# Kernel tuning notes

Hardware: AMD Instinct MI355X
Metric: run time of the kernel (lower is better)

Reference implementation:

```python
import jax, jax.numpy as jnp
import numpy as np

B, S, D, H = 2, 2048, 2048, 16
DH = D // H            # 128 head dim
QP = D // 2            # 1024 compressed q dim
KVP = (2 * D) // 3     # 1365 compressed kv dim
RD = DH // 2           # 64 rope dim
ND = DH // 2           # 64 nope dim
FF = 4 * D
THETA = 10000.0


def _ln(x, w, b, eps=1e-5):
    m = jnp.mean(x, -1, keepdims=True)
    v = jnp.mean((x - m) ** 2, -1, keepdims=True)
    return (x - m) * jax.lax.rsqrt(v + eps) * w + b


def _rotate_half(x):
    x1, x2 = jnp.split(x, 2, axis=-1)
    return jnp.concatenate([-x2, x1], axis=-1)


def setup_inputs() -> dict:
    key = jax.random.key(0)
    ks = jax.random.split(key, 9)
    rn = lambda k, shp, s: (s * jax.random.normal(k, shp)).astype(jnp.float32)
    return {
        'x': jax.random.normal(ks[0], (B, S, D), jnp.float32),
        'attn_norm_w': jnp.ones((D,), jnp.float32), 'attn_norm_b': jnp.zeros((D,), jnp.float32),
        'W_dq': rn(ks[1], (D, QP), 0.01),
        'q_ln_w': jnp.ones((QP,), jnp.float32), 'q_ln_b': jnp.zeros((QP,), jnp.float32),
        'W_uq': rn(ks[2], (QP, D), 0.01),
        'W_dkv': rn(ks[3], (D, KVP + RD), 0.01),
        'kv_ln_w': jnp.ones((KVP,), jnp.float32), 'kv_ln_b': jnp.zeros((KVP,), jnp.float32),
        'W_ukv': rn(ks[4], (KVP, D + H * ND), 0.01),
        'W_o': rn(ks[5], (D, D), 0.01),
        'ff_norm_w': jnp.ones((D,), jnp.float32), 'ff_norm_b': jnp.zeros((D,), jnp.float32),
        'W1': rn(ks[6], (D, FF), 0.02), 'b1': jnp.zeros((FF,), jnp.float32),
        'W2': rn(ks[7], (FF, D), 0.02), 'b2': jnp.zeros((D,), jnp.float32),
    }


def reference(x, attn_norm_w, attn_norm_b, W_dq, q_ln_w, q_ln_b, W_uq, W_dkv,
              kv_ln_w, kv_ln_b, W_ukv, W_o, ff_norm_w, ff_norm_b, W1, b1, W2, b2):
    # ---- pre-LN attention ----
    h = _ln(x, attn_norm_w, attn_norm_b)
    # Q path: down-proj, LN, up-proj
    cq = _ln(h @ W_dq, q_ln_w, q_ln_b)                      # [B,S,QP]
    Q = (cq @ W_uq).reshape(B, S, H, DH).transpose(0, 2, 1, 3)  # [B,H,S,DH]
    Qn, Qr = Q[..., :ND], Q[..., ND:]
    # RoPE tables: emb [S, DH/2]; take first RD/2 freqs, tile -> [1,1,S,RD]
    pos = jnp.arange(S, dtype=jnp.float32)
    freqs = 1.0 / (THETA ** (jnp.arange(0, DH, 2, dtype=jnp.float32) / DH))
    emb = pos[:, None] * freqs[None, :]
    cos = jnp.tile(jnp.cos(emb)[:, :RD // 2], (1, 2))[None, None]
    sin = jnp.tile(jnp.sin(emb)[:, :RD // 2], (1, 2))[None, None]
    Qr = Qr * cos + _rotate_half(Qr) * sin
    # KV path: joint down-proj, split latent / shared rope key
    ckv = h @ W_dkv                                          # [B,S,KVP+RD]
    kv_lora, k_rope = ckv[..., :KVP], ckv[..., KVP:]
    kv_lora = _ln(kv_lora, kv_ln_w, kv_ln_b)
    KV = (kv_lora @ W_ukv).reshape(B, S, H, DH + ND).transpose(0, 2, 1, 3)
    K, V = KV[..., :ND], KV[..., ND:]                        # K [B,H,S,ND], V [B,H,S,DH]
    Kr = k_rope[:, None]                                     # [B,1,S,RD] shared across heads
    Kr = Kr * cos + _rotate_half(Kr) * sin
    Kr = jnp.broadcast_to(Kr, (B, H, S, RD))
    q = jnp.concatenate([Qn, Qr], -1)                        # [B,H,S,DH]
    k = jnp.concatenate([K, Kr], -1)                         # [B,H,S,DH]
    scores = jnp.einsum('bhqd,bhkd->bhqk', q, k) / jnp.sqrt(jnp.float32(DH))
    mask = jnp.tril(jnp.ones((S, S), bool))
    scores = jnp.where(mask, scores, jnp.finfo(scores.dtype).min)
    attn = jax.nn.softmax(scores, axis=-1)
    o = jnp.einsum('bhqk,bhkd->bhqd', attn, V).transpose(0, 2, 1, 3).reshape(B, S, D)
    o = o @ W_o.T
    x = x + o  # dropout is identity at eval
    # ---- pre-LN MLP ----
    r = x
    h = _ln(x, ff_norm_w, ff_norm_b)
    h = jax.nn.gelu(h @ W1 + b1, approximate=False) @ W2 + b2
    return r + h, ckv
```

## Files before the change

kernel.cpp:

```cpp
#include <hip/hip_runtime.h>
#include <hip/hip_bf16.h>
#include <math.h>

#define B_ 2
#define S_ 2048
#define D_ 2048
#define H_ 16
#define DH_ 128
#define QP_ 1024
#define KVP_ 1365
#define RD_ 64
#define ND_ 64
#define FF_ 8192
#define T_ (B_*S_)
#define CKW_ (KVP_+RD_)
#define KVW_ 3072
#define KVP_PAD 1408
#define CKW_PAD 1536

typedef __attribute__((ext_vector_type(8))) short short8;
typedef __attribute__((ext_vector_type(4))) short sh4;
typedef __attribute__((ext_vector_type(4))) float floatx4;

__device__ __forceinline__ void gload_lds16(const __hip_bfloat16* g, __hip_bfloat16* l) {
    __builtin_amdgcn_global_load_lds((const __attribute__((address_space(1))) void*)g,
                                     (__attribute__((address_space(3))) void*)l, 16, 0, 0);
}
__device__ __forceinline__ short f2bs(float f) {
    __hip_bfloat16 h = __float2bfloat16(f);
    return *reinterpret_cast<short*>(&h);
}
__device__ __forceinline__ int sw(int row, int g) { return row * 64 + ((g ^ (row & 7)) << 3); }

__device__ __forceinline__ float fast_gelu(float v) {
    float x = v * 0.70710678118654752f;
    float ax = fabsf(x);
    float t = __builtin_amdgcn_rcpf(1.f + 0.3275911f * ax);
    float y = t * (0.254829592f + t * (-0.284496736f + t * (1.421413741f + t * (-1.453152027f + t * 1.061405429f))));
    float e = __expf(-ax * ax);
    float erfv = 1.f - y * e;
    erfv = copysignf(erfv, x);
    return 0.5f * v * (1.f + erfv);
}

__global__ __launch_bounds__(256) void ln_bf16(const float* __restrict__ in, int in_stride,
                                               const float* __restrict__ w, const float* __restrict__ bb,
                                               __hip_bfloat16* __restrict__ out, int out_stride, int N)
{
    int row = blockIdx.x;
    const float* ip = in + (size_t)row * in_stride;
    __hip_bfloat16* op = out + (size_t)row * out_stride;
    int tid = threadIdx.x;
    float sum = 0.f, sq = 0.f;
    for (int i = tid; i < N; i += 256) { float v = ip[i]; sum += v; sq += v * v; }
    __shared__ float s1[256], s2[256];
    s1[tid] = sum; s2[tid] = sq; __syncthreads();
    for (int s = 128; s > 0; s >>= 1) {
        if (tid < s) { s1[tid] += s1[tid + s]; s2[tid] += s2[tid + s]; }
        __syncthreads();
    }
    float mean = s1[0] / N;
    float var  = s2[0] / N - mean * mean;
    float rstd = rsqrtf(var + 1e-5f);
    for (int i = tid; i < N; i += 256) {
        float v = ip[i];
        op[i] = __float2bfloat16((v - mean) * rstd * w[i] + bb[i]);
    }
    for (int i = N + tid; i < out_stride; i += 256) op[i] = __float2bfloat16(0.f);
}

__global__ __launch_bounds__(256) void transpose_cvt(const float* __restrict__ W, __hip_bfloat16* __restrict__ Wt,
                                                     int K, int N, int Kp)
{
    __shared__ float t[32][33];
    int k0 = blockIdx.x * 32, n0 = blockIdx.y * 32;
    int tx = threadIdx.x & 31, ty = threadIdx.x >> 5;
    for (int r = ty; r < 32; r += 8) {
        int k = k0 + r, n = n0 + tx;
        t[r][tx] = (k < K && n < N) ? W[(size_t)k * N + n] : 0.f;
    }
    __syncthreads();
    for (int r = ty; r < 32; r += 8) {
        int n = n0 + r, k = k0 + tx;
        Wt[(size_t)n * Kp + k] = __float2bfloat16(t[tx][r]);
    }
}

__global__ __launch_bounds__(256) void cvt_bf16(const float* __restrict__ in, __hip_bfloat16* __restrict__ out, int n)
{
    int i = blockIdx.x * 256 + threadIdx.x;
    if (i < n) out[i] = __float2bfloat16(in[i]);
}

template<int EPI, typename CT>
__global__ __launch_bounds__(256) void gemm_bf16(const __hip_bfloat16* __restrict__ A,
                                                 const __hip_bfloat16* __restrict__ Bt,
                                                 CT* __restrict__ C, int M, int N, int Kp, int ldc,
                                                 const float* __restrict__ bias,
                                                 const float* __restrict__ resid)
{
    __shared__ __hip_bfloat16 As[128 * 64];
    __shared__ __hip_bfloat16 Bs[128 * 64];
    int tid = threadIdx.x;
    int bm = blockIdx.y * 128;
    int bn = blockIdx.x * 128;
    int wid = tid >> 6, lane = tid & 63;
    int wm = (wid >> 1) * 64, wn = (wid & 1) * 64;
    int lrow = lane & 15;
    int quad = lane >> 4;

    floatx4 acc[4][4];
    #pragma unroll
    for (int i = 0; i < 4; ++i)
        #pragma unroll
        for (int j = 0; j < 4; ++j)
            acc[i][j] = (floatx4){0.f, 0.f, 0.f, 0.f};

    for (int k0 = 0; k0 < Kp; k0 += 64) {
        #pragma unroll
        for (int it = 0; it < 4; ++it) {
            int chunk = it * 256 + tid;
            int row = chunk >> 3, g = chunk & 7;
            int col = (g ^ (row & 7)) << 3;
            gload_lds16(A + (size_t)(bm + row) * Kp + k0 + col, &As[chunk * 8]);
        }
        #pragma unroll
        for (int it = 0; it < 4; ++it) {
            int chunk = it * 256 + tid;
            int row = chunk >> 3, g = chunk & 7;
            int col = (g ^ (row & 7)) << 3;
            gload_lds16(Bt + (size_t)(bn + row) * Kp + k0 + col, &Bs[chunk * 8]);
        }
        __syncthreads();
        #pragma unroll
        for (int kk = 0; kk < 2; ++kk) {
            short8 a[4], b[4];
            #pragma unroll
            for (int i = 0; i < 4; ++i)
                a[i] = *(const short8*)&As[sw(wm + i * 16 + lrow, kk * 4 + quad)];
            #pragma unroll
            for (int j = 0; j < 4; ++j)
                b[j] = *(const short8*)&Bs[sw(wn + j * 16 + lrow, kk * 4 + quad)];
            #pragma unroll
            for (int i = 0; i < 4; ++i)
                #pragma unroll
                for (int j = 0; j < 4; ++j)
                    acc[i][j] = __builtin_amdgcn_mfma_f32_16x16x32_bf16(a[i], b[j], acc[i][j], 0, 0, 0);
        }
        __syncthreads();
    }

    int cq4 = quad * 4;
    #pragma unroll
    for (int i = 0; i < 4; ++i) {
        #pragma unroll
        for (int j = 0; j < 4; ++j) {
            int col = bn + wn + j * 16 + lrow;
            if (col >= N) continue;
            #pragma unroll
            for (int r = 0; r < 4; ++r) {
                int rowg = bm + wm + i * 16 + cq4 + r;
                float v = acc[i][j][r];
                size_t idx = (size_t)rowg * ldc + col;
                if (EPI == 1) v += resid[idx];
                if (EPI == 2) { v += bias[col]; v = fast_gelu(v); }
                if (EPI == 3) { v += bias[col]; v += ((const float*)C)[idx]; }
                C[idx] = (CT)v;
            }
        }
    }
}

__global__ __launch_bounds__(256) void rope_q_kernel(float* __restrict__ Q)
{
    int idx = blockIdx.x * 256 + threadIdx.x;
    int i = idx & 31;
    int h = (idx >> 5) & (H_ - 1);
    int t = idx >> 9;
    float f = expf(-(float)i * (9.210340371976184f / 64.0f));
    float ang = (float)(t & (S_ - 1)) * f;
    float sv, cv; sincosf(ang, &sv, &cv);
    float* p = Q + (size_t)t * D_ + h * DH_ + ND_;
    float u = p[i], v = p[i + 32];
    p[i]      = u * cv - v * sv;
    p[i + 32] = v * cv + u * sv;
}

__global__ __launch_bounds__(256) void rope_kr_bf(const float* __restrict__ ckv, __hip_bfloat16* __restrict__ kr)
{
    int idx = blockIdx.x * 256 + threadIdx.x;
    int i = idx & 31;
    int t = idx >> 5;
    float f = expf(-(float)i * (9.210340371976184f / 64.0f));
    float ang = (float)(t & (S_ - 1)) * f;
    float sv, cv; sincosf(ang, &sv, &cv);
    const float* src = ckv + (size_t)t * CKW_ + KVP_;
    float u = src[i], v = src[i + 32];
    kr[(size_t)t * RD_ + i]      = __float2bfloat16(u * cv - v * sv);
    kr[(size_t)t * RD_ + i + 32] = __float2bfloat16(v * cv + u * sv);
}

__global__ __launch_bounds__(256) void vt_pack(const __hip_bfloat16* __restrict__ kvu,
                                               __hip_bfloat16* __restrict__ Vt)
{
    int bh = blockIdx.y; int b = bh >> 4, h = bh & 15;
    int v = threadIdx.x & 127;
    int tg = blockIdx.x * 2 + (threadIdx.x >> 7);
    int t0 = tg * 8;
    short8 o;
    #pragma unroll
    for (int j = 0; j < 8; ++j) {
        __hip_bfloat16 e = kvu[(size_t)(b * S_ + t0 + j) * KVW_ + h * 192 + 64 + v];
        o[j] = *reinterpret_cast<short*>(&e);
    }
    *(short8*)&Vt[((size_t)bh * 128 + v) * S_ + t0] = o;
}

__global__ __launch_bounds__(256) void attn_mfma(const float* __restrict__ Q,
                                                 const __hip_bfloat16* __restrict__ KVU,
                                                 const __hip_bfloat16* __restrict__ KR,
                                                 const __hip_bfloat16* __restrict__ VT,
                                                 __hip_bfloat16* __restrict__ O)
{
    __shared__ __hip_bfloat16 Kls[64 * 64];
    __shared__ __hip_bfloat16 Krls[64 * 64];
    __shared__ __hip_bfloat16 Vls[128 * 64];
    __shared__ __hip_bfloat16 Pls[4 * 32 * 64];

    int tid = threadIdx.x, wid = tid >> 6, lane = tid & 63;
    int lrow = lane & 15, quad = lane >> 4;
    int kq8 = quad * 8;
    int qtile = 15 - blockIdx.x;
    int bh = blockIdx.y, b = bh >> 4, h = bh & 15;
    int q0 = qtile * 128, wq = wid * 32;

    const float scale = 0.08838834764831845f;

    short8 bq[2][2], bqr[2][2];
    #pragma unroll
    for (int n = 0; n < 2; ++n) {
        const float* qrow = Q + (size_t)(b * S_ + q0 + wq + n * 16 + lrow) * D_ + h * DH_;
        #pragma unroll
        for (int s = 0; s < 2; ++s) {
            int base = s * 32 + kq8;
            #pragma unroll
            for (int j = 0; j < 8; ++j) {
                bq[n][s][j]  = f2bs(qrow[base + j] * scale);
                bqr[n][s][j] = f2bs(qrow[64 + base + j] * scale);
            }
        }
    }

    float mstate[2] = {-INFINITY, -INFINITY};
    float lstate[2] = {0.f, 0.f};
    floatx4 acco[8][2];
    #pragma unroll
    for (int vt = 0; vt < 8; ++vt)
        #pragma unroll
        for (int n = 0; n < 2; ++n)
            acco[vt][n] = (floatx4){0.f, 0.f, 0.f, 0.f};

    int nk = qtile * 2 + 2;
    int qmax_w = q0 + wq + 31;

    for (int kt = 0; kt < nk; ++kt) {
        int k0 = kt * 64;
        #pragma unroll
        for (int it = 0; it < 2; ++it) {
            int c = it * 256 + tid;
            int row = c >> 3, g = c & 7;
            int col = ((g ^ (row & 7)) << 3);
            gload_lds16(KVU + (size_t)(b * S_ + k0 + row) * KVW_ + h * 192 + col, &Kls[c * 8]);
            gload_lds16(KR + (size_t)(b * S_ + k0 + row) * RD_ + col, &Krls[c * 8]);
        }
        #pragma unroll
        for (int it = 0; it < 4; ++it) {
            int c = it * 256 + tid;
            int row = c >> 3, g = c & 7;
            int col = ((g ^ (row & 7)) << 3);
            gload_lds16(VT + ((size_t)bh * 128 + row) * S_ + k0 + col, &Vls[c * 8]);
        }
        __syncthreads();

        if (k0 <= qmax_w) {
            floatx4 sacc[4][2];
            #pragma unroll
            for (int m = 0; m < 4; ++m)
                #pragma unroll
                for (int n = 0; n < 2; ++n)
                    sacc[m][n] = (floatx4){0.f, 0.f, 0.f, 0.f};
            #pragma unroll
            for (int m = 0; m < 4; ++m) {
                short8 ak[2], akr[2];
                #pragma unroll
                for (int s = 0; s < 2; ++s) {
                    ak[s]  = *(const short8*)&Kls[sw(m * 16 + lrow, s * 4 + quad)];
                    akr[s] = *(const short8*)&Krls[sw(m * 16 + lrow, s * 4 + quad)];
                }
                #pragma unroll
                for (int n = 0; n < 2; ++n)
                    #pragma unroll
                    for (int s = 0; s < 2; ++s) {
                        sacc[m][n] = __builtin_amdgcn_mfma_f32_16x16x32_bf16(ak[s],  bq[n][s],  sacc[m][n], 0, 0, 0);
                        sacc[m][n] = __builtin_amdgcn_mfma_f32_16x16x32_bf16(akr[s], bqr[n][s], sacc[m][n], 0, 0, 0);
                    }
            }
            #pragma unroll
            for (int n = 0; n < 2; ++n) {
                int qg = q0 + wq + n * 16 + lrow;
                float tmax = -INFINITY;
                #pragma unroll
                for (int m = 0; m < 4; ++m)
                    #pragma unroll
                    for (int r = 0; r < 4; ++r) {
                        int kg = k0 + m * 16 + quad * 4 + r;
                        if (kg > qg) sacc[m][n][r] = -1e30f;
                        tmax = fmaxf(tmax, sacc[m][n][r]);
                    }
                tmax = fmaxf(tmax, __shfl_xor(tmax, 16));
                tmax = fmaxf(tmax, __shfl_xor(tmax, 32));
                float mnew = fmaxf(mstate[n], tmax);
                float alpha = __expf(mstate[n] - mnew);
                mstate[n] = mnew;
                float ps = 0.f;
                #pragma unroll
                for (int m = 0; m < 4; ++m) {
                    sh4 pk;
                    #pragma unroll
                    for (int r = 0; r < 4; ++r) {
                        float p = __expf(sacc[m][n][r] - mnew);
                        ps += p;
                        pk[r] = f2bs(p);
                    }
                    int qloc = n * 16 + lrow;
                    int off = wid * 2048 + qloc * 64 + (((m * 2 + (quad >> 1)) ^ (lrow & 7)) << 3) + ((quad & 1) << 2);
                    *(sh4*)&Pls[off] = pk;
                }
                ps += __shfl_xor(ps, 16);
                ps += __shfl_xor(ps, 32);
                lstate[n] = lstate[n] * alpha + ps;
                #pragma unroll
                for (int vt = 0; vt < 8; ++vt)
                    #pragma unroll
                    for (int r = 0; r < 4; ++r)
                        acco[vt][n][r] *= alpha;
            }
            short8 bp[2][2];
            #pragma unroll
            for (int n = 0; n < 2; ++n)
                #pragma unroll
                for (int s = 0; s < 2; ++s)
                    bp[n][s] = *(const short8*)&Pls[wid * 2048 + sw(n * 16 + lrow, s * 4 + quad)];
            #pragma unroll
            for (int vt = 0; vt < 8; ++vt) {
                short8 av[2];
                #pragma unroll
                for (int s = 0; s < 2; ++s)
                    av[s] = *(const short8*)&Vls[sw(vt * 16 + lrow, s * 4 + quad)];
                #pragma unroll
                for (int n = 0; n < 2; ++n)
                    #pragma unroll
                    for (int s = 0; s < 2; ++s)
                        acco[vt][n] = __builtin_amdgcn_mfma_f32_16x16x32_bf16(av[s], bp[n][s], acco[vt][n], 0, 0, 0);
            }
        }
        __syncthreads();
    }

    #pragma unroll
    for (int n = 0; n < 2; ++n) {
        float inv = 1.0f / lstate[n];
        int tok = b * S_ + q0 + wq + n * 16 + lrow;
        #pragma unroll
        for (int vt = 0; vt < 8; ++vt) {
            sh4 o4;
            #pragma unroll
            for (int r = 0; r < 4; ++r) o4[r] = f2bs(acco[vt][n][r] * inv);
            *(sh4*)&O[(size_t)tok * D_ + h * DH_ + vt * 16 + quad * 4] = o4;
        }
    }
}

extern "C" void kernel_launch(void* const* d_in, const int* in_sizes, int n_in,
                              void* d_out, int out_size, void* d_ws, size_t ws_size,
                              hipStream_t stream)
{
    const float* x     = (const float*)d_in[0];
    const float* anw   = (const float*)d_in[1];
    const float* anb   = (const float*)d_in[2];
    const float* W_dq  = (const float*)d_in[3];
    const float* qlw   = (const float*)d_in[4];
    const float* qlb   = (const float*)d_in[5];
    const float* W_uq  = (const float*)d_in[6];
    const float* W_dkv = (const float*)d_in[7];
    const float* kvlw  = (const float*)d_in[8];
    const float* kvlb  = (const float*)d_in[9];
    const float* W_ukv = (const float*)d_in[10];
    const float* W_o   = (const float*)d_in[11];
    const float* fnw   = (const float*)d_in[12];
    const float* fnb   = (const float*)d_in[13];
    const float* W1    = (const float*)d_in[14];
    const float* b1    = (const float*)d_in[15];
    const float* W2    = (const float*)d_in[16];
    const float* b2    = (const float*)d_in[17];

    float* out0 = (float*)d_out;
    float* ckv  = out0 + (size_t)T_ * D_;

    float* ws = (float*)d_ws;
    float* Q  = ws;
    float* cq = Q + (size_t)T_ * D_;
    __hip_bfloat16* kvu_bf = (__hip_bfloat16*)(cq + (size_t)T_ * QP_);
    __hip_bfloat16* kr_bf  = kvu_bf + (size_t)T_ * KVW_;
    __hip_bfloat16* Vt     = kr_bf + (size_t)T_ * RD_;
    __hip_bfloat16* h_bf   = Vt + (size_t)T_ * D_;
    __hip_bfloat16* cq_bf  = h_bf + (size_t)T_ * D_;
    __hip_bfloat16* kvl_bf = cq_bf + (size_t)T_ * QP_;
    __hip_bfloat16* o_bf   = kvl_bf + (size_t)T_ * KVP_PAD;
    __hip_bfloat16* wdq_t  = o_bf + (size_t)T_ * D_;
    __hip_bfloat16* wuq_t  = wdq_t + (size_t)QP_ * D_;
    __hip_bfloat16* wdkv_t = wuq_t + (size_t)D_ * QP_;
    __hip_bfloat16* wukv_t = wdkv_t + (size_t)CKW_PAD * D_;
    __hip_bfloat16* wo_b   = wukv_t + (size_t)KVW_ * KVP_PAD;
    __hip_bfloat16* w1_t   = wo_b + (size_t)D_ * D_;
    __hip_bfloat16* w2_t   = w1_t + (size_t)FF_ * D_;
    __hip_bfloat16* ff1_bf = (__hip_bfloat16*)ws;

    dim3 blk(256);

    { dim3 g(D_ / 32, QP_ / 32);       transpose_cvt<<<g, blk, 0, stream>>>(W_dq,  wdq_t,  D_, QP_, D_); }
    { dim3 g(QP_ / 32, D_ / 32);       transpose_cvt<<<g, blk, 0, stream>>>(W_uq,  wuq_t,  QP_, D_, QP_); }
    { dim3 g(D_ / 32, CKW_PAD / 32);   transpose_cvt<<<g, blk, 0, stream>>>(W_dkv, wdkv_t, D_, CKW_, D_); }
    { dim3 g(KVP_PAD / 32, KVW_ / 32); transpose_cvt<<<g, blk, 0, stream>>>(W_ukv, wukv_t, KVP_, KVW_, KVP_PAD); }
    { int n = D_ * D_;                 cvt_bf16<<<(n + 255) / 256, blk, 0, stream>>>(W_o, wo_b, n); }
    { dim3 g(D_ / 32, FF_ / 32);       transpose_cvt<<<g, blk, 0, stream>>>(W1, w1_t, D_, FF_, D_); }
    { dim3 g(FF_ / 32, D_ / 32);       transpose_cvt<<<g, blk, 0, stream>>>(W2, w2_t, FF_, D_, FF_); }

    ln_bf16<<<T_, blk, 0, stream>>>(x, D_, anw, anb, h_bf, D_, D_);
    { dim3 g(QP_ / 128, T_ / 128);
      gemm_bf16<0, float><<<g, blk, 0, stream>>>(h_bf, wdq_t, cq, T_, QP_, D_, QP_, nullptr, nullptr); }
    ln_bf16<<<T_, blk, 0, stream>>>(cq, QP_, qlw, qlb, cq_bf, QP_, QP_);
    { dim3 g(D_ / 128, T_ / 128);
      gemm_bf16<0, float><<<g, blk, 0, stream>>>(cq_bf, wuq_t, Q, T_, D_, QP_, D_, nullptr, nullptr); }
    rope_q_kernel<<<(T_ * H_ * 32) / 256, blk, 0, stream>>>(Q);
    { dim3 g(CKW_PAD / 128, T_ / 128);
      gemm_bf16<0, float><<<g, blk, 0, stream>>>(h_bf, wdkv_t, ckv, T_, CKW_, D_, CKW_, nullptr, nullptr); }
    ln_bf16<<<T_, blk, 0, stream>>>(ckv, CKW_, kvlw, kvlb, kvl_bf, KVP_PAD, KVP_);
    { dim3 g(KVW_ / 128, T_ / 128);
      gemm_bf16<0, __hip_bfloat16><<<g, blk, 0, stream>>>(kvl_bf, wukv_t, kvu_bf, T_, KVW_, KVP_PAD, KVW_, nullptr, nullptr); }
    rope_kr_bf<<<(T_ * 32) / 256, blk, 0, stream>>>(ckv, kr_bf);
    { dim3 g(S_ / 16, B_ * H_);
      vt_pack<<<g, blk, 0, stream>>>(kvu_bf, Vt); }
    { dim3 g(16, B_ * H_);
      attn_mfma<<<g, blk, 0, stream>>>(Q, kvu_bf, kr_bf, Vt, o_bf); }
    { dim3 g(D_ / 128, T_ / 128);
      gemm_bf16<1, float><<<g, blk, 0, stream>>>(o_bf, wo_b, out0, T_, D_, D_, D_, nullptr, x); }
    ln_bf16<<<T_, blk, 0, stream>>>(out0, D_, fnw, fnb, h_bf, D_, D_);
    { dim3 g(FF_ / 128, T_ / 128);
      gemm_bf16<2, __hip_bfloat16><<<g, blk, 0, stream>>>(h_bf, w1_t, ff1_bf, T_, FF_, D_, FF_, b1, nullptr); }
    { dim3 g(D_ / 128, T_ / 128);
      gemm_bf16<3, float><<<g, blk, 0, stream>>>(ff1_bf, w2_t, out0, T_, D_, FF_, D_, b2, nullptr); }
}
```

Measured before the change: 1.138 ms.

## Add 256x256 eight-phase pipelined bf16 GEMM with XCD-aware tile remap

Adds a 512-thread GEMM kernel with 256x256 output tiles. It double-buffers A and B in LDS, interleaves global-to-LDS staging with MFMA quarter-blocks across eight barrier-separated phases, and raises MFMA wave priority. Block indices are remapped so consecutive tiles land on the same XCD for L2 reuse. It replaces the 128x128 GEMM for the up-projections, output projection and both MLP GEMMs, aiming for more reuse per LDS load and better overlap of loads with compute. The large tiles, 128 KB of LDS and many accumulator registers can limit occupancy, and tail handling for N not divisible by 256 is not guarded.

New measurement: 1.508 ms. +32.5%, slower.

```diff
diff --git a/kernel.cpp b/kernel.cpp
--- a/kernel.cpp
+++ b/kernel.cpp
@@ -169,6 +169,166 @@
             }
         }
     }
+}
+
+#define BAR8() __builtin_amdgcn_s_barrier()
+#define SCB8() __builtin_amdgcn_sched_barrier(0)
+#define GATE8(nw) asm volatile("s_waitcnt vmcnt(" #nw ")" ::: "memory")
+
+template<int EPI, typename CT>
+__global__ __launch_bounds__(512, 2) void gemm_8ph(const __hip_bfloat16* __restrict__ A,
+                                                   const __hip_bfloat16* __restrict__ Bt,
+                                                   CT* __restrict__ C, int M, int N, int Kp, int ldc,
+                                                   const float* __restrict__ bias,
+                                                   const float* __restrict__ resid)
+{
+    __shared__ __hip_bfloat16 As[2][16384];
+    __shared__ __hip_bfloat16 Bs[2][16384];
+
+    int tid = threadIdx.x;
+    int wid = tid >> 6, lane = tid & 63;
+    int lrow = lane & 15, quad = lane >> 4;
+    int awm = (wid >> 2) * 128;
+    int bwn = (wid & 3) * 64;
+
+    int gx = gridDim.x;
+    int nwg = gx * gridDim.y;
+    int o = blockIdx.y * gx + blockIdx.x;
+    int q8 = nwg >> 3, r8 = nwg & 7;
+    int xcd = o & 7, oi = o >> 3;
+    int s = (xcd < r8 ? xcd * (q8 + 1) : r8 * (q8 + 1) + (xcd - r8) * q8) + oi;
+    int bm = (s / gx) * 256, bn = (s % gx) * 256;
+
+    const __hip_bfloat16* Abm = A  + (size_t)bm * Kp;
+    const __hip_bfloat16* Bbn = Bt + (size_t)bn * Kp;
+
+    int drow = tid >> 3;
+    int csw  = ((tid & 7) ^ (drow & 7)) << 3;
+    int ldst = tid * 8;
+
+#define STAGE8(srcbase, k0v, dst) do { \
+    gload_lds16((srcbase) + (size_t)drow * Kp + (k0v) + csw, (dst) + ldst); \
+    gload_lds16((srcbase) + (size_t)(drow + 64) * Kp + (k0v) + csw, (dst) + 4096 + ldst); \
+  } while (0)
+
+    int abase = awm + lrow;
+    int bbase = bwn + lrow;
+    int k0off = ((quad       ^ (lrow & 7)) << 3);
+    int k1off = (((4 + quad) ^ (lrow & 7)) << 3);
+
+    short8 af[8][2], bfr[4][2];
+    floatx4 acc[8][4];
+    #pragma unroll
+    for (int m = 0; m < 8; ++m)
+        #pragma unroll
+        for (int n = 0; n < 4; ++n)
+            acc[m][n] = (floatx4){0.f, 0.f, 0.f, 0.f};
+
+#define READ_A8(bufp, mh) do { \
+    _Pragma("unroll") \
+    for (int m = 0; m < 4; ++m) { \
+      const __hip_bfloat16* p_ = (bufp) + (abase + ((mh)*4 + m) * 16) * 64; \
+      af[(mh)*4 + m][0] = *(const short8*)(p_ + k0off); \
+      af[(mh)*4 + m][1] = *(const short8*)(p_ + k1off); \
+    } } while (0)
+
+#define READ_B8(bufp, nh) do { \
+    _Pragma("unroll") \
+    for (int n = 0; n < 2; ++n) { \
+      const __hip_bfloat16* p_ = (bufp) + (bbase + ((nh)*2 + n) * 16) * 64; \
+      bfr[(nh)*2 + n][0] = *(const short8*)(p_ + k0off); \
+      bfr[(nh)*2 + n][1] = *(const short8*)(p_ + k1off); \
+    } } while (0)
+
+#define QMFMA8(mh, nh) do { \
+    __builtin_amdgcn_s_setprio(1); \
+    _Pragma("unroll") \
+    for (int kk = 0; kk < 2; ++kk) \
+      _Pragma("unroll") \
+      for (int m = 0; m < 4; ++m) \
+        _Pragma("unroll") \
+        for (int n = 0; n < 2; ++n) \
+          acc[(mh)*4 + m][(nh)*2 + n] = __builtin_amdgcn_mfma_f32_16x16x32_bf16( \
+              af[(mh)*4 + m][kk], bfr[(nh)*2 + n][kk], acc[(mh)*4 + m][(nh)*2 + n], 0, 0, 0); \
+    __builtin_amdgcn_s_setprio(0); \
+  } while (0)
+
+    STAGE8(Abm,                   0,  &As[0][0]);
+    STAGE8(Abm + (size_t)128*Kp,  0,  &As[0][8192]);
+    STAGE8(Bbn,                   0,  &Bs[0][0]);
+    STAGE8(Bbn + (size_t)128*Kp,  0,  &Bs[0][8192]);
+    STAGE8(Abm,                   64, &As[1][0]);
+    STAGE8(Abm + (size_t)128*Kp,  64, &As[1][8192]);
+    GATE8(4); SCB8(); BAR8();
+
+    int NT = Kp >> 6;
+    #pragma unroll 1
+    for (int t = 0; t < NT; t += 2) {
+        int kn = (t + 1) << 6;
+        int k2 = ((t + 2 < NT) ? t + 2 : NT - 1) << 6;
+        int k3 = ((t + 3 < NT) ? t + 3 : NT - 1) << 6;
+
+        STAGE8(Bbn, kn, &Bs[1][0]);
+        READ_A8(&As[0][0], 0); READ_B8(&Bs[0][0], 0);
+        SCB8(); BAR8();
+        QMFMA8(0, 0);
+        SCB8(); BAR8();
+        STAGE8(Bbn + (size_t)128*Kp, kn, &Bs[1][8192]);
+        READ_A8(&As[0][0], 1); READ_B8(&Bs[0][0], 1);
+        SCB8(); BAR8();
+        QMFMA8(1, 1);
+        SCB8(); BAR8();
+        STAGE8(Abm, k2, &As[0][0]);
+        SCB8(); BAR8();
+        QMFMA8(0, 1);
+        SCB8(); BAR8();
+        STAGE8(Abm + (size_t)128*Kp, k2, &As[0][8192]);
+        SCB8(); BAR8();
+        QMFMA8(1, 0);
+        GATE8(4); SCB8(); BAR8();
+        STAGE8(Bbn, k2, &Bs[0][0]);
+        READ_A8(&As[1][0], 0); READ_B8(&Bs[1][0], 0);
+        SCB8(); BAR8();
+        QMFMA8(0, 0);
+        SCB8(); BAR8();
+        STAGE8(Bbn + (size_t)128*Kp, k2, &Bs[0][8192]);
+        READ_A8(&As[1][0], 1); READ_B8(&Bs[1][0], 1);
+        SCB8(); BAR8();
+        QMFMA8(1, 1);
+        SCB8(); BAR8();
+        STAGE8(Abm, k3, &As[1][0]);
+        SCB8(); BAR8();
+        QMFMA8(0, 1);
+        SCB8(); BAR8();
+        STAGE8(Abm + (size_t)128*Kp, k3, &As[1][8192]);
+        SCB8(); BAR8();
+        QMFMA8(1, 0);
+        GATE8(4); SCB8(); BAR8();
+    }
+    asm volatile("s_waitcnt vmcnt(0)" ::: "memory");
+
+    int cq4 = quad * 4;
+    #pragma unroll
+    for (int m = 0; m < 8; ++m) {
+        int rowg = bm + awm + m * 16 + cq4;
+        #pragma unroll
+        for (int n = 0; n < 4; ++n) {
+            int col = bn + bwn + n * 16 + lrow;
+            #pragma unroll
+            for (int r = 0; r < 4; ++r) {
+                float v = acc[m][n][r];
+                size_t idx = (size_t)(rowg + r) * ldc + col;
+                if (EPI == 1) v += resid[idx];
+                if (EPI == 2) { v += bias[col]; v = fast_gelu(v); }
+                if (EPI == 3) { v += bias[col]; v += ((const float*)C)[idx]; }
+                C[idx] = (CT)v;
+            }
+        }
+    }
+#undef STAGE8
+#undef READ_A8
+#undef READ_B8
+#undef QMFMA8
 }
 
 __global__ __launch_bounds__(256) void rope_q_kernel(float* __restrict__ Q)
@@ -427,6 +587,7 @@
     __hip_bfloat16* ff1_bf = (__hip_bfloat16*)ws;
 
     dim3 blk(256);
+    dim3 blk8(512);
 
     { dim3 g(D_ / 32, QP_ / 32);       transpose_cvt<<<g, blk, 0, stream>>>(W_dq,  wdq_t,  D_, QP_, D_); }
     { dim3 g(QP_ / 32, D_ / 32);       transpose_cvt<<<g, blk, 0, stream>>>(W_uq,  wuq_t,  QP_, D_, QP_); }
@@ -440,24 +601,24 @@
     { dim3 g(QP_ / 128, T_ / 128);
       gemm_bf16<0, float><<<g, blk, 0, stream>>>(h_bf, wdq_t, cq, T_, QP_, D_, QP_, nullptr, nullptr); }
     ln_bf16<<<T_, blk, 0, stream>>>(cq, QP_, qlw, qlb, cq_bf, QP_, QP_);
-    { dim3 g(D_ / 128, T_ / 128);
-      gemm_bf16<0, float><<<g, blk, 0, stream>>>(cq_bf, wuq_t, Q, T_, D_, QP_, D_, nullptr, nullptr); }
+    { dim3 g(D_ / 256, T_ / 256);
+      gemm_8ph<0, float><<<g, blk8, 0, stream>>>(cq_bf, wuq_t, Q, T_, D_, QP_, D_, nullptr, nullptr); }
     rope_q_kernel<<<(T_ * H_ * 32) / 256, blk, 0, stream>>>(Q);
     { dim3 g(CKW_PAD / 128, T_ / 128);
       gemm_bf16<0, float><<<g, blk, 0, stream>>>(h_bf, wdkv_t, ckv, T_, CKW_, D_, CKW_, nullptr, nullptr); }
     ln_bf16<<<T_, blk, 0, stream>>>(ckv, CKW_, kvlw, kvlb, kvl_bf, KVP_PAD, KVP_);
-    { dim3 g(KVW_ / 128, T_ / 128);
-      gemm_bf16<0, __hip_bfloat16><<<g, blk, 0, stream>>>(kvl_bf, wukv_t, kvu_bf, T_, KVW_, KVP_PAD, KVW_, nullptr, nullptr); }
+    { dim3 g(KVW_ / 256, T_ / 256);
+      gemm_8ph<0, __hip_bfloat16><<<g, blk8, 0, stream>>>(kvl_bf, wukv_t, kvu_bf, T_, KVW_, KVP_PAD, KVW_, nullptr, nullptr); }
     rope_kr_bf<<<(T_ * 32) / 256, blk, 0, stream>>>(ckv, kr_bf);
     { dim3 g(S_ / 16, B_ * H_);
       vt_pack<<<g, blk, 0, stream>>>(kvu_bf, Vt); }
     { dim3 g(16, B_ * H_);
       attn_mfma<<<g, blk, 0, stream>>>(Q, kvu_bf, kr_bf, Vt, o_bf); }
-    { dim3 g(D_ / 128, T_ / 128);
-      gemm_bf16<1, float><<<g, blk, 0, stream>>>(o_bf, wo_b, out0, T_, D_, D_, D_, nullptr, x); }
+    { dim3 g(D_ / 256, T_ / 256);
+      gemm_8ph<1, float><<<g, blk8, 0, stream>>>(o_bf, wo_b, out0, T_, D_, D_, D_, nullptr, x); }
     ln_bf16<<<T_, blk, 0, stream>>>(out0, D_, fnw, fnb, h_bf, D_, D_);
-    { dim3 g(FF_ / 128, T_ / 128);
-      gemm_bf16<2, __hip_bfloat16><<<g, blk, 0, stream>>>(h_bf, w1_t, ff1_bf, T_, FF_, D_, FF_, b1, nullptr); }
-    { dim3 g(D_ / 128, T_ / 128);
-      gemm_bf16<3, float><<<g, blk, 0, stream>>>(ff1_bf, w2_t, out0, T_, D_, FF_, D_, b2, nullptr); }
-}
+    { dim3 g(FF_ / 256, T_ / 256);
+      gemm_8ph<2, __hip_bfloat16><<<g, blk8, 0, stream>>>(h_bf, w1_t, ff1_bf, T_, FF_, D_, FF_, b1, nullptr); }
+    { dim3 g(D_ / 256, T_ / 256);
+      gemm_8ph<3, float><<<g, blk8, 0, stream>>>(ff1_bf, w2_t, out0, T_, D_, FF_, D_, b2, nullptr); }
+}
```
